# Kernel tuning notes

Measured on AMD Instinct MI355X. Metric: run time of the kernel, lower is better.

The kernel has to match this reference:

```python
import jax, jax.numpy as jnp
import numpy as np
from itertools import permutations

S_SPK, B, T, C = 2, 16, 300, 3000
NUM_STATES, NUM_ARCS = 400, 1200
DEN_STATES, DEN_ARCS = 3000, 60000
DEN_SCALE = 1.0
NEG = -1e30


def setup_inputs() -> dict:
    key = jax.random.key(0)
    ks = jax.random.split(key, 14)
    est_llhs = jax.nn.log_softmax(
        jax.random.normal(ks[0], (S_SPK, B, T, C), jnp.float32), axis=-1)
    seqlengths = jax.random.randint(ks[1], (B,), T // 2, T + 1, jnp.int32)
    num_src = jax.random.randint(ks[2], (S_SPK, B, NUM_ARCS), 0, NUM_STATES, jnp.int32)
    num_dst = jax.random.randint(ks[3], (S_SPK, B, NUM_ARCS), 0, NUM_STATES, jnp.int32)
    num_label = jax.random.randint(ks[4], (S_SPK, B, NUM_ARCS), 0, C, jnp.int32)
    num_weight = -2.0 * jax.random.uniform(ks[5], (S_SPK, B, NUM_ARCS), jnp.float32)
    num_start = -5.0 * jax.random.uniform(ks[6], (S_SPK, B, NUM_STATES), jnp.float32)
    num_final = -5.0 * jax.random.uniform(ks[7], (S_SPK, B, NUM_STATES), jnp.float32)
    den_src = jax.random.randint(ks[8], (DEN_ARCS,), 0, DEN_STATES, jnp.int32)
    den_dst = jax.random.randint(ks[9], (DEN_ARCS,), 0, DEN_STATES, jnp.int32)
    den_label = jax.random.randint(ks[10], (DEN_ARCS,), 0, C, jnp.int32)
    den_weight = -2.0 * jax.random.uniform(ks[11], (DEN_ARCS,), jnp.float32)
    den_start = -5.0 * jax.random.uniform(ks[12], (DEN_STATES,), jnp.float32)
    den_final = -5.0 * jax.random.uniform(ks[13], (DEN_STATES,), jnp.float32)
    return dict(est_llhs=est_llhs, seqlengths=seqlengths,
                num_src=num_src, num_dst=num_dst, num_label=num_label,
                num_weight=num_weight, num_start=num_start, num_final=num_final,
                den_src=den_src, den_dst=den_dst, den_label=den_label,
                den_weight=den_weight, den_start=den_start, den_final=den_final)


def _segment_lse(scores, idx, n):
    # stable log-sum-exp scatter over destination states
    m = jax.ops.segment_max(scores, idx, num_segments=n)
    m_safe = jnp.where(jnp.isfinite(m), m, 0.0)
    s = jax.ops.segment_sum(jnp.exp(scores - m_safe[idx]), idx, num_segments=n)
    s_safe = jnp.where(s > 0, s, 1.0)
    return jnp.where(s > 0, m_safe + jnp.log(s_safe), NEG)


def _fsa_logZ(llh, seqlen, src, dst, lab, w, start, final):
    # forward algorithm: alpha_{t+1}[dst] = LSE_arcs(alpha_t[src] + w + llh[t, lab])
    n = start.shape[0]
    mask = jnp.arange(llh.shape[0]) < seqlen

    def step(alpha, inp):
        t_llh, valid = inp
        scores = alpha[src] + w + t_llh[lab]
        new_alpha = _segment_lse(scores, dst, n)
        return jnp.where(valid, new_alpha, alpha), None

    alpha, _ = jax.lax.scan(step, start, (llh, mask))
    return jax.scipy.special.logsumexp(alpha + final)


_num_logZ = jax.vmap(_fsa_logZ)  # all graph args batched over B
_den_logZ = jax.vmap(_fsa_logZ, in_axes=(0, 0, None, None, None, None, None, None))


def reference(est_llhs, seqlengths, num_src, num_dst, num_label, num_weight,
              num_start, num_final, den_src, den_dst, den_label, den_weight,
              den_start, den_final):
    n_spk = est_llhs.shape[0]
    bsz = est_llhs.shape[1]
    # denominator log-marginal per (batch, speaker): [B, S]
    den_llh = jnp.stack(
        [_den_logZ(est_llhs[s], seqlengths, den_src, den_dst, den_label,
                   den_weight, den_start, den_final) for s in range(n_spk)], axis=1)
    # numerator log-marginals for every permutation: [P, B, S]
    perms = list(permutations(range(n_spk)))
    num_llh_perms = jnp.stack([
        jnp.stack([_num_logZ(est_llhs[s], seqlengths, num_src[p], num_dst[p],
                             num_label[p], num_weight[p], num_start[p], num_final[p])
                   for s, p in enumerate(perm)], axis=1)
        for perm in perms], axis=0)
    # best permutation per utterance
    idxs = jnp.argmax(num_llh_perms.sum(axis=2), axis=0)  # [B]
    num_llh = jnp.take_along_axis(
        num_llh_perms, jnp.broadcast_to(idxs[None, :, None], (1, bsz, n_spk)),
        axis=0)[0]  # [B, S]
    loss = -(num_llh - DEN_SCALE * den_llh)
    return loss.sum()
```

## Files before the change

### kernel.cpp

```cpp
#include <hip/hip_runtime.h>
#include <hip/hip_bf16.h>

#define S_SPK 2
#define BATCH 16
#define TMAX 300
#define CLASSES 3000
#define NUM_STATES 400
#define NUM_ARCS 1200
#define DEN_STATES 3000
#define DEN_ARCS 60000

#define BLK 768
#define NWAVE 12
#define KCH 6
#define CHST 500
#define NSEQ 32
#define NUM_CAP_G 2400
#define NGRAPH 32

#define WS_DEN_ARCS   0
#define WS_NUM_ARCS   576000
#define WS_DEN_CNT    1190400
#define WS_DEN_R      1202400
#define WS_DEN_CUR    1214416
#define WS_NUM_CNT    1226416
#define WS_NUM_R      1277616
#define WS_NUM_CUR    1328944
#define WS_GALPHA     1380144
#define WS_FLAGS      2148144
#define WS_BINS       2156336
#define WS_DEN_Z      2156592
#define WS_NUM_Z      2156720
#define WS_BINCUR     2156976
#define WS_PI         2157232
#define WS_INV        2169232
#define WS_ZERO_INTS  (2156592 / 4)

__global__ void zero_ws(int* __restrict__ p, int n) {
    int i = blockIdx.x * blockDim.x + threadIdx.x;
    for (; i < n; i += gridDim.x * blockDim.x) p[i] = 0;
}

__global__ void hist_all(const int* __restrict__ dden, int* __restrict__ dcnt,
                         const int* __restrict__ dnum, int* __restrict__ ncnt) {
    int i = blockIdx.x * blockDim.x + threadIdx.x;
    if (i < DEN_ARCS) atomicAdd(&dcnt[dden[i]], 1);
    if (i < NGRAPH * NUM_ARCS) {
        int g = i / NUM_ARCS;
        atomicAdd(&ncnt[g * NUM_STATES + dnum[i]], 1);
    }
}

__global__ void prep_den(const int* __restrict__ cnt, int* __restrict__ pi,
                         int* __restrict__ inv, int* __restrict__ R) {
    __shared__ int bins[64], bcur[64], sc[1024];
    const int tid = threadIdx.x;

    if (tid < 64) bins[tid] = 0;
    __syncthreads();

    int c0 = 0, c1 = 0, c2 = 0;
    if (tid < 1000) {
        c0 = cnt[3 * tid]; c1 = cnt[3 * tid + 1]; c2 = cnt[3 * tid + 2];
        atomicAdd(&bins[min(c0, 63)], 1);
        atomicAdd(&bins[min(c1, 63)], 1);
        atomicAdd(&bins[min(c2, 63)], 1);
    }
    __syncthreads();

    if (tid < 64) {
        int sum = 0;
        for (int b = 63; b > tid; --b) sum += bins[b];
        bcur[tid] = sum;
    }
    __syncthreads();

    if (tid < 1000) {
        int cc[3] = { c0, c1, c2 };
        #pragma unroll
        for (int j = 0; j < 3; ++j) {
            int c = min(cc[j], 63);
            int rank = atomicAdd(&bcur[c], 1);
            int pos = (rank % KCH) * CHST + rank / KCH;
            pi[3 * tid + j] = pos;
            inv[pos] = 3 * tid + j;
        }
    }
    __syncthreads();

    int d0 = 0, d1 = 0, d2 = 0, p0 = 0, p1 = 0, p2 = 0, pg = 0;
    if (tid < 1000) {
        d0 = cnt[inv[3 * tid]]; d1 = cnt[inv[3 * tid + 1]]; d2 = cnt[inv[3 * tid + 2]];
        p0 = (d0 + 3) & ~3; p1 = (d1 + 3) & ~3; p2 = (d2 + 3) & ~3;
        pg = p0 + p1 + p2;
    }
    sc[tid] = pg; __syncthreads();
    for (int o = 1; o < 1024; o <<= 1) {
        int v = (tid >= o) ? sc[tid - o] : 0;
        __syncthreads(); sc[tid] += v; __syncthreads();
    }
    int ex = sc[tid] - pg;
    if (tid < 1000) {
        R[3 * tid] = ex; R[3 * tid + 1] = ex + p0; R[3 * tid + 2] = ex + p0 + p1;
    }
    if (tid == 1000) R[3000] = ex;
}

__global__ void scan_num(const int* __restrict__ cnt, int* __restrict__ R) {
    __shared__ int sc[512];
    int g = blockIdx.x, tid = threadIdx.x;
    int c = 0, pg = 0;
    if (tid < NUM_STATES) { c = cnt[g * NUM_STATES + tid]; pg = (c + 3) & ~3; }
    sc[tid] = pg; __syncthreads();
    for (int o = 1; o < 512; o <<= 1) {
        int v = (tid >= o) ? sc[tid - o] : 0;
        __syncthreads(); sc[tid] += v; __syncthreads();
    }
    int ex = sc[tid] - pg;
    if (tid <= NUM_STATES) R[g * (NUM_STATES + 1) + tid] = ex;
}

__global__ void scat_all(
    const int* __restrict__ dsrc, const int* __restrict__ ddst,
    const int* __restrict__ dlab, const float* __restrict__ dw,
    const int* __restrict__ dR, int* __restrict__ dcur,
    const int* __restrict__ pi, int2* __restrict__ dout,
    const int* __restrict__ nsrc, const int* __restrict__ ndst,
    const int* __restrict__ nlab, const float* __restrict__ nw,
    const int* __restrict__ nR, int* __restrict__ ncur, int2* __restrict__ nout)
{
    int i = blockIdx.x * blockDim.x + threadIdx.x;
    if (i < DEN_ARCS) {
        int dpos = pi[ddst[i]];
        int spos = pi[dsrc[i]];
        int pos = dR[dpos] + atomicAdd(&dcur[dpos], 1);
        dout[pos] = make_int2(spos | (dlab[i] << 16), __float_as_int(__expf(dw[i])));
    }
    if (i < NGRAPH * NUM_ARCS) {
        int g = i / NUM_ARCS;
        int d = ndst[i];
        int pos = nR[g * (NUM_STATES + 1) + d] + atomicAdd(&ncur[g * NUM_STATES + d], 1);
        nout[g * NUM_CAP_G + pos] =
            make_int2(nsrc[i] | (nlab[i] << 16), __float_as_int(__expf(nw[i])));
    }
}

__device__ __forceinline__ void num_fwd(
    const int* __restrict__ R, const int2* __restrict__ arcs,
    const float* __restrict__ start, const float* __restrict__ fin,
    const float* __restrict__ est, int L, float* __restrict__ out,
    float* A0, float* A1, float* p, float* red)
{
    const int tid = threadIdx.x, lane = tid & 63, wid = tid >> 6;

    if (tid < NUM_STATES) A0[tid] = __expf(start[tid]);

    int rs = 0, re = 0;
    if (tid < NUM_STATES) { rs = R[tid]; re = R[tid + 1]; }

    float l0 = est[tid], l1 = est[tid + 768], l2 = est[tid + 1536];
    float l3 = (tid < 696) ? est[tid + 2304] : 0.f;

    float c = 1.f, OFF = 0.f, pend = 0.f;
    const int4* arcs4 = (const int4*)arcs;

    for (int t = 0; t < L; ++t) {
        OFF += pend;
        p[tid] = __expf(l0) * c;        p[tid + 768] = __expf(l1) * c;
        p[tid + 1536] = __expf(l2) * c;
        if (tid < 696) p[tid + 2304] = __expf(l3) * c;
        {
            const float* nr = est + (size_t)((t + 1 < L) ? (t + 1) : t) * CLASSES;
            l0 = nr[tid]; l1 = nr[tid + 768]; l2 = nr[tid + 1536];
            if (tid < 696) l3 = nr[tid + 2304];
        }
        __syncthreads();

        const float* Ac = (t & 1) ? A1 : A0;
        float*       An = (t & 1) ? A0 : A1;
        float a0 = 0.f;
        for (int r = rs; r < re; r += 4) {
            int4 q0 = arcs4[(r >> 1)];
            int4 q1 = arcs4[(r >> 1) + 1];
            a0 += Ac[q0.x & 0xffff] * p[((unsigned)q0.x) >> 16] * __int_as_float(q0.y);
            a0 += Ac[q0.z & 0xffff] * p[((unsigned)q0.z) >> 16] * __int_as_float(q0.w);
            a0 += Ac[q1.x & 0xffff] * p[((unsigned)q1.x) >> 16] * __int_as_float(q1.y);
            a0 += Ac[q1.z & 0xffff] * p[((unsigned)q1.z) >> 16] * __int_as_float(q1.w);
        }
        float mymax = 0.f;
        if (tid < NUM_STATES) { An[tid] = a0; mymax = a0; }
        #pragma unroll
        for (int o = 32; o > 0; o >>= 1) mymax = fmaxf(mymax, __shfl_down(mymax, o, 64));
        if (lane == 0) red[wid] = mymax;
        __syncthreads();
        float M = red[0];
        #pragma unroll
        for (int k = 1; k < NWAVE; ++k) M = fmaxf(M, red[k]);
        M = fmaxf(M, 1e-37f);
        c = 1.0f / M;
        pend = __logf(M);
    }

    const float* Af = (L & 1) ? A1 : A0;
    float fs = 0.f;
    if (tid < NUM_STATES) fs = Af[tid] * __expf(fin[tid]);
    __syncthreads();
    #pragma unroll
    for (int o = 32; o > 0; o >>= 1) fs += __shfl_down(fs, o, 64);
    if (lane == 0) red[wid] = fs;
    __syncthreads();
    if (tid == 0) {
        float s = 0.f;
        #pragma unroll
        for (int k = 0; k < NWAVE; ++k) s += red[k];
        out[0] = OFF + __logf(s);
    }
}

__global__ __launch_bounds__(BLK) void forward_kernel(
    const float* __restrict__ est, const int* __restrict__ seqlen,
    const int2* __restrict__ den_arcs, const int* __restrict__ den_R,
    const float* __restrict__ den_start, const float* __restrict__ den_final,
    const int* __restrict__ den_inv,
    const int2* __restrict__ num_arcs, const int* __restrict__ num_R,
    const float* __restrict__ num_start, const float* __restrict__ num_final,
    float* __restrict__ galpha,
    float* __restrict__ den_z, float* __restrict__ num_z)
{
    __shared__ float S1[2][DEN_STATES];
    __shared__ float S2[2][CLASSES];
    __shared__ float red[2][16];

    const int blk = blockIdx.x;
    const int tid = threadIdx.x, lane = tid & 63, wid = tid >> 6;

    if (blk < KCH * NSEQ) {
        const int seq = blk & 31;
        const int chunk = blk >> 5;
        const int b = seq & 15;
        const int L = seqlen[b];
        const float* est_base = est + (size_t)seq * TMAX * CLASSES;
        const int base = chunk * CHST;
        unsigned* gaU = (unsigned*)galpha;

        int rs = 0, re = 0;
        if (tid < CHST) { rs = den_R[base + tid]; re = den_R[base + tid + 1]; }
        const int4* arcs4 = (const int4*)den_arcs;
        const int4* ap = arcs4 + (rs >> 1);
        const int n4 = (re - rs) >> 2;

        float l0 = est_base[tid], l1 = est_base[tid + 768], l2 = est_base[tid + 1536];
        float l3 = (tid < 696) ? est_base[tid + 2304] : 0.f;

        float OFF = 0.f;

        for (int t = 0; t < L; ++t) {
            const int cur = t & 1;
            float* S1c = S1[cur];
            float* S2c = S2[cur];

            S2c[tid] = __expf(l0); S2c[tid + 768] = __expf(l1); S2c[tid + 1536] = __expf(l2);
            if (tid < 696) S2c[tid + 2304] = __expf(l3);
            {
                const float* nr = est_base + (size_t)((t + 1 < L) ? (t + 1) : t) * CLASSES;
                l0 = nr[tid]; l1 = nr[tid + 768]; l2 = nr[tid + 1536];
                if (tid < 696) l3 = nr[tid + 2304];
            }

            int4 a0 = ap[0], a1 = ap[1], b0 = ap[2], b1 = ap[3];

            if (t == 0) {
                S1c[tid]        = __expf(den_start[den_inv[tid]]);
                S1c[tid + 768]  = __expf(den_start[den_inv[tid + 768]]);
                S1c[tid + 1536] = __expf(den_start[den_inv[tid + 1536]]);
                if (tid < 696) S1c[tid + 2304] = __expf(den_start[den_inv[tid + 2304]]);
            } else {
                const unsigned tg = (unsigned)((t - 1) % 3) + 1u;
                const unsigned* gp = gaU + ((size_t)seq * 2 + ((t - 1) & 1)) * DEN_STATES;
                unsigned u0, u1, u2, u3 = tg;
                for (;;) {
                    u0 = __hip_atomic_load(gp + tid,        __ATOMIC_RELAXED, __HIP_MEMORY_SCOPE_AGENT);
                    u1 = __hip_atomic_load(gp + tid + 768,  __ATOMIC_RELAXED, __HIP_MEMORY_SCOPE_AGENT);
                    u2 = __hip_atomic_load(gp + tid + 1536, __ATOMIC_RELAXED, __HIP_MEMORY_SCOPE_AGENT);
                    if (tid < 696)
                        u3 = __hip_atomic_load(gp + tid + 2304, __ATOMIC_RELAXED, __HIP_MEMORY_SCOPE_AGENT);
                    if ((((u0 & 3u) == tg) && ((u1 & 3u) == tg)) &&
                        (((u2 & 3u) == tg) && ((u3 & 3u) == tg))) break;
                    __builtin_amdgcn_s_sleep(1);
                }
                float x0 = __uint_as_float(u0 & ~3u);
                float x1 = __uint_as_float(u1 & ~3u);
                float x2 = __uint_as_float(u2 & ~3u);
                float x3 = (tid < 696) ? __uint_as_float(u3 & ~3u) : 0.f;
                S1c[tid] = x0; S1c[tid + 768] = x1; S1c[tid + 1536] = x2;
                if (tid < 696) S1c[tid + 2304] = x3;
                float mymax = fmaxf(fmaxf(x0, x1), fmaxf(x2, x3));
                #pragma unroll
                for (int o = 32; o > 0; o >>= 1)
                    mymax = fmaxf(mymax, __shfl_down(mymax, o, 64));
                if (lane == 0) red[cur][wid] = mymax;
            }

            __syncthreads();

            float cM = 1.0f;
            if (t) {
                const float4* r4 = (const float4*)red[cur];
                float4 ra = r4[0], rb = r4[1], rc = r4[2];
                float M = fmaxf(fmaxf(fmaxf(ra.x, ra.y), fmaxf(ra.z, ra.w)),
                         fmaxf(fmaxf(fmaxf(rb.x, rb.y), fmaxf(rb.z, rb.w)),
                               fmaxf(fmaxf(rc.x, rc.y), fmaxf(rc.z, rc.w))));
                M = fmaxf(M, 1e-37f);
                cM = 1.0f / M;
                OFF += __logf(M);
            }

            float acc = 0.f;
            for (int i = 0; i < n4; ++i) {
                int4 p0 = ap[2 * i + 4], p1 = ap[2 * i + 5];
                acc += S1c[a0.x & 0xffff] * S2c[((unsigned)a0.x) >> 16] * __int_as_float(a0.y);
                acc += S1c[a0.z & 0xffff] * S2c[((unsigned)a0.z) >> 16] * __int_as_float(a0.w);
                acc += S1c[a1.x & 0xffff] * S2c[((unsigned)a1.x) >> 16] * __int_as_float(a1.y);
                acc += S1c[a1.z & 0xffff] * S2c[((unsigned)a1.z) >> 16] * __int_as_float(a1.w);
                a0 = b0; a1 = b1; b0 = p0; b1 = p1;
            }

            if (tid < CHST) {
                unsigned uv = (__float_as_uint(acc * cM) & ~3u) | ((unsigned)(t % 3) + 1u);
                __hip_atomic_store(gaU + ((size_t)seq * 2 + cur) * DEN_STATES + base + tid,
                                   uv, __ATOMIC_RELAXED, __HIP_MEMORY_SCOPE_AGENT);
            }
            asm volatile("" ::: "memory");
        }

        if (chunk == 0) {
            __syncthreads();
            const unsigned tg = (unsigned)((L - 1) % 3) + 1u;
            const unsigned* gp = gaU + ((size_t)seq * 2 + ((L - 1) & 1)) * DEN_STATES;
            unsigned u0, u1, u2, u3 = tg;
            for (;;) {
                u0 = __hip_atomic_load(gp + tid,        __ATOMIC_RELAXED, __HIP_MEMORY_SCOPE_AGENT);
                u1 = __hip_atomic_load(gp + tid + 768,  __ATOMIC_RELAXED, __HIP_MEMORY_SCOPE_AGENT);
                u2 = __hip_atomic_load(gp + tid + 1536, __ATOMIC_RELAXED, __HIP_MEMORY_SCOPE_AGENT);
                if (tid < 696)
                    u3 = __hip_atomic_load(gp + tid + 2304, __ATOMIC_RELAXED, __HIP_MEMORY_SCOPE_AGENT);
                if ((((u0 & 3u) == tg) && ((u1 & 3u) == tg)) &&
                    (((u2 & 3u) == tg) && ((u3 & 3u) == tg))) break;
                __builtin_amdgcn_s_sleep(1);
            }
            float fs = __uint_as_float(u0 & ~3u) * __expf(den_final[den_inv[tid]])
                     + __uint_as_float(u1 & ~3u) * __expf(den_final[den_inv[tid + 768]])
                     + __uint_as_float(u2 & ~3u) * __expf(den_final[den_inv[tid + 1536]]);
            if (tid < 696)
                fs += __uint_as_float(u3 & ~3u) * __expf(den_final[den_inv[tid + 2304]]);
            #pragma unroll
            for (int o = 32; o > 0; o >>= 1) fs += __shfl_down(fs, o, 64);
            if (lane == 0) red[0][wid] = fs;
            __syncthreads();
            if (tid == 0) {
                float s = 0.f;
                #pragma unroll
                for (int k = 0; k < NWAVE; ++k) s += red[0][k];
                den_z[seq] = OFF + __logf(s);
            }
        }
    } else {
        const int q = blk - KCH * NSEQ;
        const int b = q & 15;
        const int sp = q >> 4;
        const int s = sp >> 1, pp = sp & 1;
        const int L = seqlen[b];
        const int g = pp * BATCH + b;
        num_fwd(num_R + (size_t)g * (NUM_STATES + 1),
                num_arcs + (size_t)g * NUM_CAP_G,
                num_start + (size_t)g * NUM_STATES,
                num_final + (size_t)g * NUM_STATES,
                est + (size_t)(s * BATCH + b) * TMAX * CLASSES, L, &num_z[q],
                &S1[0][0], &S1[0][1536], &S2[0][0], &red[0][0]);
    }
}

__global__ void loss_kernel(const float* __restrict__ den_z,
                            const float* __restrict__ num_z,
                            float* __restrict__ out)
{
    int tid = threadIdx.x;
    float l = 0.f;
    if (tid < BATCH) {
        int b = tid;
        float z00 = num_z[(0 * 2 + 0) * BATCH + b];
        float z01 = num_z[(0 * 2 + 1) * BATCH + b];
        float z10 = num_z[(1 * 2 + 0) * BATCH + b];
        float z11 = num_z[(1 * 2 + 1) * BATCH + b];
        float perm0 = z00 + z11;
        float perm1 = z01 + z10;
        float n0, n1;
        if (perm0 >= perm1) { n0 = z00; n1 = z11; }
        else                { n0 = z01; n1 = z10; }
        l = -(n0 - den_z[0 * BATCH + b]) - (n1 - den_z[1 * BATCH + b]);
    }
    #pragma unroll
    for (int o = 32; o > 0; o >>= 1) l += __shfl_down(l, o, 64);
    if (tid == 0) out[0] = l;
}

extern "C" void kernel_launch(void* const* d_in, const int* in_sizes, int n_in,
                              void* d_out, int out_size, void* d_ws, size_t ws_size,
                              hipStream_t stream) {
    const float* est        = (const float*)d_in[0];
    const int*   seqlen     = (const int*)d_in[1];
    const int*   num_src    = (const int*)d_in[2];
    const int*   num_dst    = (const int*)d_in[3];
    const int*   num_label  = (const int*)d_in[4];
    const float* num_weight = (const float*)d_in[5];
    const float* num_start  = (const float*)d_in[6];
    const float* num_final  = (const float*)d_in[7];
    const int*   den_src    = (const int*)d_in[8];
    const int*   den_dst    = (const int*)d_in[9];
    const int*   den_label  = (const int*)d_in[10];
    const float* den_weight = (const float*)d_in[11];
    const float* den_start  = (const float*)d_in[12];
    const float* den_final  = (const float*)d_in[13];

    char* ws = (char*)d_ws;
    int2*     den_arcs = (int2*)(ws + WS_DEN_ARCS);
    int2*     num_arcs = (int2*)(ws + WS_NUM_ARCS);
    int*      den_cnt  = (int*)(ws + WS_DEN_CNT);
    int*      den_R    = (int*)(ws + WS_DEN_R);
    int*      den_cur  = (int*)(ws + WS_DEN_CUR);
    int*      num_cnt  = (int*)(ws + WS_NUM_CNT);
    int*      num_R    = (int*)(ws + WS_NUM_R);
    int*      num_cur  = (int*)(ws + WS_NUM_CUR);
    float*    galpha   = (float*)(ws + WS_GALPHA);
    float*    den_z    = (float*)(ws + WS_DEN_Z);
    float*    num_z    = (float*)(ws + WS_NUM_Z);
    int*      pi       = (int*)(ws + WS_PI);
    int*      inv      = (int*)(ws + WS_INV);

    zero_ws<<<512, 256, 0, stream>>>((int*)ws, WS_ZERO_INTS);
    hist_all<<<(DEN_ARCS + 255) / 256, 256, 0, stream>>>(den_dst, den_cnt,
                                                         num_dst, num_cnt);
    prep_den<<<1, 1024, 0, stream>>>(den_cnt, pi, inv, den_R);
    scan_num<<<NGRAPH, 512, 0, stream>>>(num_cnt, num_R);
    scat_all<<<(DEN_ARCS + 255) / 256, 256, 0, stream>>>(
        den_src, den_dst, den_label, den_weight, den_R, den_cur, pi, den_arcs,
        num_src, num_dst, num_label, num_weight, num_R, num_cur, num_arcs);

    forward_kernel<<<KCH * NSEQ + S_SPK * S_SPK * BATCH, BLK, 0, stream>>>(
        est, seqlen, den_arcs, den_R, den_start, den_final, inv,
        num_arcs, num_R, num_start, num_final,
        galpha, den_z, num_z);

    loss_kernel<<<1, 64, 0, stream>>>(den_z, num_z, (float*)d_out);
}
```

Measured before the change: 1.563 ms.

## Pair speaker sequences per block sharing arc loads; split den states into 12 chunks

Each denominator block now processes two sequences that share a batch index and the same graph (speaker 0 and speaker 1). Each arc record is loaded once and applied to both sequences' alpha and emission tables. The state range is split into 12 chunks of 250 instead of 6 chunks of 500, so the block count stays at 192 while per-thread arc work halves. This cuts redundant arc-list global traffic but doubles LDS use (about 96KB), may lower occupancy, and makes each block's spin-wait depend on both sequences becoming ready.

```diff
diff --git a/kernel.cpp b/kernel.cpp
--- a/kernel.cpp
+++ b/kernel.cpp
@@ -12,8 +12,9 @@
 
 #define BLK 768
 #define NWAVE 12
-#define KCH 6
-#define CHST 500
+#define KCH 12
+#define CHST 250
+#define NPAIR 16
 #define NSEQ 32
 #define NUM_CAP_G 2400
 #define NGRAPH 32
@@ -27,11 +28,8 @@
 #define WS_NUM_R      1277616
 #define WS_NUM_CUR    1328944
 #define WS_GALPHA     1380144
-#define WS_FLAGS      2148144
-#define WS_BINS       2156336
 #define WS_DEN_Z      2156592
 #define WS_NUM_Z      2156720
-#define WS_BINCUR     2156976
 #define WS_PI         2157232
 #define WS_INV        2169232
 #define WS_ZERO_INTS  (2156592 / 4)
@@ -227,19 +225,22 @@
     float* __restrict__ galpha,
     float* __restrict__ den_z, float* __restrict__ num_z)
 {
-    __shared__ float S1[2][DEN_STATES];
-    __shared__ float S2[2][CLASSES];
-    __shared__ float red[2][16];
+    __shared__ float S1A[2][DEN_STATES];
+    __shared__ float S1B[2][DEN_STATES];
+    __shared__ float S2A[2][CLASSES];
+    __shared__ float S2B[2][CLASSES];
+    __shared__ float redA[2][16], redB[2][16];
 
     const int blk = blockIdx.x;
     const int tid = threadIdx.x, lane = tid & 63, wid = tid >> 6;
 
-    if (blk < KCH * NSEQ) {
-        const int seq = blk & 31;
-        const int chunk = blk >> 5;
-        const int b = seq & 15;
-        const int L = seqlen[b];
-        const float* est_base = est + (size_t)seq * TMAX * CLASSES;
+    if (blk < KCH * NPAIR) {
+        const int q = blk & 15;
+        const int chunk = blk >> 4;
+        const int seqA = q, seqB = q + 16;
+        const int L = seqlen[q];
+        const float* estA = est + (size_t)seqA * TMAX * CLASSES;
+        const float* estB = est + (size_t)seqB * TMAX * CLASSES;
         const int base = chunk * CHST;
         unsigned* gaU = (unsigned*)galpha;
 
@@ -249,86 +250,141 @@
         const int4* ap = arcs4 + (rs >> 1);
         const int n4 = (re - rs) >> 2;
 
-        float l0 = est_base[tid], l1 = est_base[tid + 768], l2 = est_base[tid + 1536];
-        float l3 = (tid < 696) ? est_base[tid + 2304] : 0.f;
-
-        float OFF = 0.f;
+        float lA0 = estA[tid], lA1 = estA[tid + 768], lA2 = estA[tid + 1536];
+        float lA3 = (tid < 696) ? estA[tid + 2304] : 0.f;
+        float lB0 = estB[tid], lB1 = estB[tid + 768], lB2 = estB[tid + 1536];
+        float lB3 = (tid < 696) ? estB[tid + 2304] : 0.f;
+
+        float OFFA = 0.f, OFFB = 0.f;
 
         for (int t = 0; t < L; ++t) {
             const int cur = t & 1;
-            float* S1c = S1[cur];
-            float* S2c = S2[cur];
-
-            S2c[tid] = __expf(l0); S2c[tid + 768] = __expf(l1); S2c[tid + 1536] = __expf(l2);
-            if (tid < 696) S2c[tid + 2304] = __expf(l3);
+            float* S1Ac = S1A[cur]; float* S1Bc = S1B[cur];
+            float* S2Ac = S2A[cur]; float* S2Bc = S2B[cur];
+
+            S2Ac[tid] = __expf(lA0); S2Ac[tid + 768] = __expf(lA1);
+            S2Ac[tid + 1536] = __expf(lA2);
+            if (tid < 696) S2Ac[tid + 2304] = __expf(lA3);
+            S2Bc[tid] = __expf(lB0); S2Bc[tid + 768] = __expf(lB1);
+            S2Bc[tid + 1536] = __expf(lB2);
+            if (tid < 696) S2Bc[tid + 2304] = __expf(lB3);
             {
-                const float* nr = est_base + (size_t)((t + 1 < L) ? (t + 1) : t) * CLASSES;
-                l0 = nr[tid]; l1 = nr[tid + 768]; l2 = nr[tid + 1536];
-                if (tid < 696) l3 = nr[tid + 2304];
-            }
-
-            int4 a0 = ap[0], a1 = ap[1], b0 = ap[2], b1 = ap[3];
+                const size_t row = (size_t)((t + 1 < L) ? (t + 1) : t) * CLASSES;
+                const float* nrA = estA + row; const float* nrB = estB + row;
+                lA0 = nrA[tid]; lA1 = nrA[tid + 768]; lA2 = nrA[tid + 1536];
+                if (tid < 696) lA3 = nrA[tid + 2304];
+                lB0 = nrB[tid]; lB1 = nrB[tid + 768]; lB2 = nrB[tid + 1536];
+                if (tid < 696) lB3 = nrB[tid + 2304];
+            }
+
+            int4 d0 = ap[0], d1 = ap[1], e0 = ap[2], e1 = ap[3];
 
             if (t == 0) {
-                S1c[tid]        = __expf(den_start[den_inv[tid]]);
-                S1c[tid + 768]  = __expf(den_start[den_inv[tid + 768]]);
-                S1c[tid + 1536] = __expf(den_start[den_inv[tid + 1536]]);
-                if (tid < 696) S1c[tid + 2304] = __expf(den_start[den_inv[tid + 2304]]);
+                float v0 = __expf(den_start[den_inv[tid]]);
+                float v1 = __expf(den_start[den_inv[tid + 768]]);
+                float v2 = __expf(den_start[den_inv[tid + 1536]]);
+                S1Ac[tid] = v0;        S1Bc[tid] = v0;
+                S1Ac[tid + 768] = v1;  S1Bc[tid + 768] = v1;
+                S1Ac[tid + 1536] = v2; S1Bc[tid + 1536] = v2;
+                if (tid < 696) {
+                    float v3 = __expf(den_start[den_inv[tid + 2304]]);
+                    S1Ac[tid + 2304] = v3; S1Bc[tid + 2304] = v3;
+                }
             } else {
                 const unsigned tg = (unsigned)((t - 1) % 3) + 1u;
-                const unsigned* gp = gaU + ((size_t)seq * 2 + ((t - 1) & 1)) * DEN_STATES;
-                unsigned u0, u1, u2, u3 = tg;
+                const unsigned* gpA = gaU + ((size_t)seqA * 2 + ((t - 1) & 1)) * DEN_STATES;
+                const unsigned* gpB = gaU + ((size_t)seqB * 2 + ((t - 1) & 1)) * DEN_STATES;
+                unsigned uA0, uA1, uA2, uA3 = tg, uB0, uB1, uB2, uB3 = tg;
                 for (;;) {
-                    u0 = __hip_atomic_load(gp + tid,        __ATOMIC_RELAXED, __HIP_MEMORY_SCOPE_AGENT);
-                    u1 = __hip_atomic_load(gp + tid + 768,  __ATOMIC_RELAXED, __HIP_MEMORY_SCOPE_AGENT);
-                    u2 = __hip_atomic_load(gp + tid + 1536, __ATOMIC_RELAXED, __HIP_MEMORY_SCOPE_AGENT);
-                    if (tid < 696)
-                        u3 = __hip_atomic_load(gp + tid + 2304, __ATOMIC_RELAXED, __HIP_MEMORY_SCOPE_AGENT);
-                    if ((((u0 & 3u) == tg) && ((u1 & 3u) == tg)) &&
-                        (((u2 & 3u) == tg) && ((u3 & 3u) == tg))) break;
+                    uA0 = __hip_atomic_load(gpA + tid,        __ATOMIC_RELAXED, __HIP_MEMORY_SCOPE_AGENT);
+                    uA1 = __hip_atomic_load(gpA + tid + 768,  __ATOMIC_RELAXED, __HIP_MEMORY_SCOPE_AGENT);
+                    uA2 = __hip_atomic_load(gpA + tid + 1536, __ATOMIC_RELAXED, __HIP_MEMORY_SCOPE_AGENT);
+                    uB0 = __hip_atomic_load(gpB + tid,        __ATOMIC_RELAXED, __HIP_MEMORY_SCOPE_AGENT);
+                    uB1 = __hip_atomic_load(gpB + tid + 768,  __ATOMIC_RELAXED, __HIP_MEMORY_SCOPE_AGENT);
+                    uB2 = __hip_atomic_load(gpB + tid + 1536, __ATOMIC_RELAXED, __HIP_MEMORY_SCOPE_AGENT);
+                    if (tid < 696) {
+                        uA3 = __hip_atomic_load(gpA + tid + 2304, __ATOMIC_RELAXED, __HIP_MEMORY_SCOPE_AGENT);
+                        uB3 = __hip_atomic_load(gpB + tid + 2304, __ATOMIC_RELAXED, __HIP_MEMORY_SCOPE_AGENT);
+                    }
+                    bool okA = ((uA0 & 3u) == tg) && ((uA1 & 3u) == tg) &&
+                               ((uA2 & 3u) == tg) && ((uA3 & 3u) == tg);
+                    bool okB = ((uB0 & 3u) == tg) && ((uB1 & 3u) == tg) &&
+                               ((uB2 & 3u) == tg) && ((uB3 & 3u) == tg);
+                    if (okA && okB) break;
                     __builtin_amdgcn_s_sleep(1);
                 }
-                float x0 = __uint_as_float(u0 & ~3u);
-                float x1 = __uint_as_float(u1 & ~3u);
-                float x2 = __uint_as_float(u2 & ~3u);
-                float x3 = (tid < 696) ? __uint_as_float(u3 & ~3u) : 0.f;
-                S1c[tid] = x0; S1c[tid + 768] = x1; S1c[tid + 1536] = x2;
-                if (tid < 696) S1c[tid + 2304] = x3;
-                float mymax = fmaxf(fmaxf(x0, x1), fmaxf(x2, x3));
+                float xA0 = __uint_as_float(uA0 & ~3u), xA1 = __uint_as_float(uA1 & ~3u);
+                float xA2 = __uint_as_float(uA2 & ~3u);
+                float xA3 = (tid < 696) ? __uint_as_float(uA3 & ~3u) : 0.f;
+                float xB0 = __uint_as_float(uB0 & ~3u), xB1 = __uint_as_float(uB1 & ~3u);
+                float xB2 = __uint_as_float(uB2 & ~3u);
+                float xB3 = (tid < 696) ? __uint_as_float(uB3 & ~3u) : 0.f;
+                S1Ac[tid] = xA0; S1Ac[tid + 768] = xA1; S1Ac[tid + 1536] = xA2;
+                S1Bc[tid] = xB0; S1Bc[tid + 768] = xB1; S1Bc[tid + 1536] = xB2;
+                if (tid < 696) { S1Ac[tid + 2304] = xA3; S1Bc[tid + 2304] = xB3; }
+                float mA = fmaxf(fmaxf(xA0, xA1), fmaxf(xA2, xA3));
+                float mB = fmaxf(fmaxf(xB0, xB1), fmaxf(xB2, xB3));
                 #pragma unroll
-                for (int o = 32; o > 0; o >>= 1)
-                    mymax = fmaxf(mymax, __shfl_down(mymax, o, 64));
-                if (lane == 0) red[cur][wid] = mymax;
+                for (int o = 32; o > 0; o >>= 1) {
+                    mA = fmaxf(mA, __shfl_down(mA, o, 64));
+                    mB = fmaxf(mB, __shfl_down(mB, o, 64));
+                }
+                if (lane == 0) { redA[cur][wid] = mA; redB[cur][wid] = mB; }
             }
 
             __syncthreads();
 
-            float cM = 1.0f;
+            float cMA = 1.0f, cMB = 1.0f;
             if (t) {
-                const float4* r4 = (const float4*)red[cur];
-                float4 ra = r4[0], rb = r4[1], rc = r4[2];
-                float M = fmaxf(fmaxf(fmaxf(ra.x, ra.y), fmaxf(ra.z, ra.w)),
-                         fmaxf(fmaxf(fmaxf(rb.x, rb.y), fmaxf(rb.z, rb.w)),
-                               fmaxf(fmaxf(rc.x, rc.y), fmaxf(rc.z, rc.w))));
-                M = fmaxf(M, 1e-37f);
-                cM = 1.0f / M;
-                OFF += __logf(M);
-            }
-
-            float acc = 0.f;
+                const float4* rA = (const float4*)redA[cur];
+                const float4* rB = (const float4*)redB[cur];
+                float4 a4 = rA[0], b4 = rA[1], c4 = rA[2];
+                float MA = fmaxf(fmaxf(fmaxf(a4.x, a4.y), fmaxf(a4.z, a4.w)),
+                          fmaxf(fmaxf(fmaxf(b4.x, b4.y), fmaxf(b4.z, b4.w)),
+                                fmaxf(fmaxf(c4.x, c4.y), fmaxf(c4.z, c4.w))));
+                a4 = rB[0]; b4 = rB[1]; c4 = rB[2];
+                float MB = fmaxf(fmaxf(fmaxf(a4.x, a4.y), fmaxf(a4.z, a4.w)),
+                          fmaxf(fmaxf(fmaxf(b4.x, b4.y), fmaxf(b4.z, b4.w)),
+                                fmaxf(fmaxf(c4.x, c4.y), fmaxf(c4.z, c4.w))));
+                MA = fmaxf(MA, 1e-37f); MB = fmaxf(MB, 1e-37f);
+                cMA = 1.0f / MA; cMB = 1.0f / MB;
+                OFFA += __logf(MA); OFFB += __logf(MB);
+            }
+
+            float accA = 0.f, accB = 0.f;
             for (int i = 0; i < n4; ++i) {
                 int4 p0 = ap[2 * i + 4], p1 = ap[2 * i + 5];
-                acc += S1c[a0.x & 0xffff] * S2c[((unsigned)a0.x) >> 16] * __int_as_float(a0.y);
-                acc += S1c[a0.z & 0xffff] * S2c[((unsigned)a0.z) >> 16] * __int_as_float(a0.w);
-                acc += S1c[a1.x & 0xffff] * S2c[((unsigned)a1.x) >> 16] * __int_as_float(a1.y);
-                acc += S1c[a1.z & 0xffff] * S2c[((unsigned)a1.z) >> 16] * __int_as_float(a1.w);
-                a0 = b0; a1 = b1; b0 = p0; b1 = p1;
+                {
+                    int s = d0.x & 0xffff; unsigned c = ((unsigned)d0.x) >> 16;
+                    float w = __int_as_float(d0.y);
+                    accA += S1Ac[s] * S2Ac[c] * w; accB += S1Bc[s] * S2Bc[c] * w;
+                }
+                {
+                    int s = d0.z & 0xffff; unsigned c = ((unsigned)d0.z) >> 16;
+                    float w = __int_as_float(d0.w);
+                    accA += S1Ac[s] * S2Ac[c] * w; accB += S1Bc[s] * S2Bc[c] * w;
+                }
+                {
+                    int s = d1.x & 0xffff; unsigned c = ((unsigned)d1.x) >> 16;
+                    float w = __int_as_float(d1.y);
+                    accA += S1Ac[s] * S2Ac[c] * w; accB += S1Bc[s] * S2Bc[c] * w;
+                }
+                {
+                    int s = d1.z & 0xffff; unsigned c = ((unsigned)d1.z) >> 16;
+                    float w = __int_as_float(d1.w);
+                    accA += S1Ac[s] * S2Ac[c] * w; accB += S1Bc[s] * S2Bc[c] * w;
+                }
+                d0 = e0; d1 = e1; e0 = p0; e1 = p1;
             }
 
             if (tid < CHST) {
-                unsigned uv = (__float_as_uint(acc * cM) & ~3u) | ((unsigned)(t % 3) + 1u);
-                __hip_atomic_store(gaU + ((size_t)seq * 2 + cur) * DEN_STATES + base + tid,
-                                   uv, __ATOMIC_RELAXED, __HIP_MEMORY_SCOPE_AGENT);
+                const unsigned tag = (unsigned)(t % 3) + 1u;
+                unsigned uvA = (__float_as_uint(accA * cMA) & ~3u) | tag;
+                unsigned uvB = (__float_as_uint(accB * cMB) & ~3u) | tag;
+                __hip_atomic_store(gaU + ((size_t)seqA * 2 + cur) * DEN_STATES + base + tid,
+                                   uvA, __ATOMIC_RELAXED, __HIP_MEMORY_SCOPE_AGENT);
+                __hip_atomic_store(gaU + ((size_t)seqB * 2 + cur) * DEN_STATES + base + tid,
+                                   uvB, __ATOMIC_RELAXED, __HIP_MEMORY_SCOPE_AGENT);
             }
             asm volatile("" ::: "memory");
         }
@@ -336,36 +392,58 @@
         if (chunk == 0) {
             __syncthreads();
             const unsigned tg = (unsigned)((L - 1) % 3) + 1u;
-            const unsigned* gp = gaU + ((size_t)seq * 2 + ((L - 1) & 1)) * DEN_STATES;
-            unsigned u0, u1, u2, u3 = tg;
+            const unsigned* gpA = gaU + ((size_t)seqA * 2 + ((L - 1) & 1)) * DEN_STATES;
+            const unsigned* gpB = gaU + ((size_t)seqB * 2 + ((L - 1) & 1)) * DEN_STATES;
+            unsigned uA0, uA1, uA2, uA3 = tg, uB0, uB1, uB2, uB3 = tg;
             for (;;) {
-                u0 = __hip_atomic_load(gp + tid,        __ATOMIC_RELAXED, __HIP_MEMORY_SCOPE_AGENT);
-                u1 = __hip_atomic_load(gp + tid + 768,  __ATOMIC_RELAXED, __HIP_MEMORY_SCOPE_AGENT);
-                u2 = __hip_atomic_load(gp + tid + 1536, __ATOMIC_RELAXED, __HIP_MEMORY_SCOPE_AGENT);
-                if (tid < 696)
-                    u3 = __hip_atomic_load(gp + tid + 2304, __ATOMIC_RELAXED, __HIP_MEMORY_SCOPE_AGENT);
-                if ((((u0 & 3u) == tg) && ((u1 & 3u) == tg)) &&
-                    (((u2 & 3u) == tg) && ((u3 & 3u) == tg))) break;
+                uA0 = __hip_atomic_load(gpA + tid,        __ATOMIC_RELAXED, __HIP_MEMORY_SCOPE_AGENT);
+                uA1 = __hip_atomic_load(gpA + tid + 768,  __ATOMIC_RELAXED, __HIP_MEMORY_SCOPE_AGENT);
+                uA2 = __hip_atomic_load(gpA + tid + 1536, __ATOMIC_RELAXED, __HIP_MEMORY_SCOPE_AGENT);
+                uB0 = __hip_atomic_load(gpB + tid,        __ATOMIC_RELAXED, __HIP_MEMORY_SCOPE_AGENT);
+                uB1 = __hip_atomic_load(gpB + tid + 768,  __ATOMIC_RELAXED, __HIP_MEMORY_SCOPE_AGENT);
+                uB2 = __hip_atomic_load(gpB + tid + 1536, __ATOMIC_RELAXED, __HIP_MEMORY_SCOPE_AGENT);
+                if (tid < 696) {
+                    uA3 = __hip_atomic_load(gpA + tid + 2304, __ATOMIC_RELAXED, __HIP_MEMORY_SCOPE_AGENT);
+                    uB3 = __hip_atomic_load(gpB + tid + 2304, __ATOMIC_RELAXED, __HIP_MEMORY_SCOPE_AGENT);
+                }
+                bool okA = ((uA0 & 3u) == tg) && ((uA1 & 3u) == tg) &&
+                           ((uA2 & 3u) == tg) && ((uA3 & 3u) == tg);
+                bool okB = ((uB0 & 3u) == tg) && ((uB1 & 3u) == tg) &&
+                           ((uB2 & 3u) == tg) && ((uB3 & 3u) == tg);
+                if (okA && okB) break;
                 __builtin_amdgcn_s_sleep(1);
             }
-            float fs = __uint_as_float(u0 & ~3u) * __expf(den_final[den_inv[tid]])
-                     + __uint_as_float(u1 & ~3u) * __expf(den_final[den_inv[tid + 768]])
-                     + __uint_as_float(u2 & ~3u) * __expf(den_final[den_inv[tid + 1536]]);
-            if (tid < 696)
-                fs += __uint_as_float(u3 & ~3u) * __expf(den_final[den_inv[tid + 2304]]);
+            float f0 = __expf(den_final[den_inv[tid]]);
+            float f1 = __expf(den_final[den_inv[tid + 768]]);
+            float f2 = __expf(den_final[den_inv[tid + 1536]]);
+            float fsA = __uint_as_float(uA0 & ~3u) * f0
+                      + __uint_as_float(uA1 & ~3u) * f1
+                      + __uint_as_float(uA2 & ~3u) * f2;
+            float fsB = __uint_as_float(uB0 & ~3u) * f0
+                      + __uint_as_float(uB1 & ~3u) * f1
+                      + __uint_as_float(uB2 & ~3u) * f2;
+            if (tid < 696) {
+                float f3 = __expf(den_final[den_inv[tid + 2304]]);
+                fsA += __uint_as_float(uA3 & ~3u) * f3;
+                fsB += __uint_as_float(uB3 & ~3u) * f3;
+            }
             #pragma unroll
-            for (int o = 32; o > 0; o >>= 1) fs += __shfl_down(fs, o, 64);
-            if (lane == 0) red[0][wid] = fs;
+            for (int o = 32; o > 0; o >>= 1) {
+                fsA += __shfl_down(fsA, o, 64);
+                fsB += __shfl_down(fsB, o, 64);
+            }
+            if (lane == 0) { redA[0][wid] = fsA; redB[0][wid] = fsB; }
             __syncthreads();
             if (tid == 0) {
-                float s = 0.f;
+                float sA = 0.f, sB = 0.f;
                 #pragma unroll
-                for (int k = 0; k < NWAVE; ++k) s += red[0][k];
-                den_z[seq] = OFF + __logf(s);
+                for (int k = 0; k < NWAVE; ++k) { sA += redA[0][k]; sB += redB[0][k]; }
+                den_z[seqA] = OFFA + __logf(sA);
+                den_z[seqB] = OFFB + __logf(sB);
             }
         }
     } else {
-        const int q = blk - KCH * NSEQ;
+        const int q = blk - KCH * NPAIR;
         const int b = q & 15;
         const int sp = q >> 4;
         const int s = sp >> 1, pp = sp & 1;
@@ -376,7 +454,7 @@
                 num_start + (size_t)g * NUM_STATES,
                 num_final + (size_t)g * NUM_STATES,
                 est + (size_t)(s * BATCH + b) * TMAX * CLASSES, L, &num_z[q],
-                &S1[0][0], &S1[0][1536], &S2[0][0], &red[0][0]);
+                &S1A[0][0], &S1A[0][1536], &S2A[0][0], &redA[0][0]);
     }
 }
 
@@ -446,7 +524,7 @@
         den_src, den_dst, den_label, den_weight, den_R, den_cur, pi, den_arcs,
         num_src, num_dst, num_label, num_weight, num_R, num_cur, num_arcs);
 
-    forward_kernel<<<KCH * NSEQ + S_SPK * S_SPK * BATCH, BLK, 0, stream>>>(
+    forward_kernel<<<KCH * NPAIR + S_SPK * S_SPK * BATCH, BLK, 0, stream>>>(
         est, seqlen, den_arcs, den_R, den_start, den_final, inv,
         num_arcs, num_R, num_start, num_final,
         galpha, den_z, num_z);
```

New measurement: 1.906 ms. 1.22x slower.
